# Optimization experiments

Hardware: AMD Instinct MI355X
Metric: run time of the kernel (lower is better)

## Reference

```python
import jax, jax.numpy as jnp
import numpy as np

B, C, H, W = 4, 128, 128, 128
SPHERE_SIZE, NUM_VOTES, NUM_PTS = 32768, 32, 4096
HW = H * W


def setup_inputs() -> dict:
    key = jax.random.key(0)
    k1, k2, k3, k4 = jax.random.split(key, 4)
    x = jax.random.normal(k1, (B, C, H, W), dtype=jnp.float32)
    vote_index = jax.random.randint(k2, (SPHERE_SIZE, NUM_VOTES), 0, HW, dtype=jnp.int32)
    vote_weight = jax.random.uniform(k3, (SPHERE_SIZE, NUM_VOTES), dtype=jnp.float32)
    inds = jax.random.randint(k4, (B, NUM_PTS), 0, SPHERE_SIZE, dtype=jnp.int64)
    return {"x": x, "vote_index": vote_index, "vote_weight": vote_weight, "inds": inds}


def reference(x, vote_index, vote_weight, inds):
    b, c, h, w = x.shape
    xf = x.reshape(b, c, h * w)                      # [B, C, HW]
    idx = jnp.take(vote_index, inds, axis=0)          # [B, P, V] flat HT indices
    wts = jnp.take(vote_weight, inds, axis=0)         # [B, P, V] vote weights

    def per_batch(xb, ib, wb):
        # xb: [C, HW], ib/wb: [P, V]
        g = jnp.take(xb, ib, axis=1)                  # [C, P, V] gather
        return jnp.einsum('cpv,pv->cp', g, wb)        # weighted vote accumulation

    return jax.vmap(per_batch)(xf, idx, wts)          # [B, C, P]
```

## Files before the change

### kernel.cpp

```cpp
#include <hip/hip_runtime.h>

constexpr int BB  = 4;
constexpr int CC  = 128;
constexpr int HWW = 16384;
constexpr int NV  = 32;
constexpr int NP  = 4096;
constexpr int PT  = 8;
constexpr int GT  = 128;

__global__ __launch_bounds__(256) void transpose_k(const float* __restrict__ x,
                                                   float* __restrict__ xt) {
  __shared__ float tile[32][33];
  const int b   = blockIdx.z;
  const int hw0 = blockIdx.x * 32;
  const int c0  = blockIdx.y * 32;
  const int tx  = threadIdx.x;
  const int ty  = threadIdx.y;
  const float* xb  = x  + (size_t)b * CC * HWW;
  float*       xtb = xt + (size_t)b * HWW * CC;
#pragma unroll
  for (int j = 0; j < 4; ++j)
    tile[ty + j * 8][tx] = xb[(size_t)(c0 + ty + j * 8) * HWW + hw0 + tx];
  __syncthreads();
#pragma unroll
  for (int j = 0; j < 4; ++j)
    xtb[(size_t)(hw0 + ty + j * 8) * CC + c0 + tx] = tile[tx][ty + j * 8];
}

__global__ __launch_bounds__(GT, 4) void gather_k(const float* __restrict__ xt,
                                                  const int* __restrict__ vote_index,
                                                  const float* __restrict__ vote_weight,
                                                  const int* __restrict__ inds,
                                                  float* __restrict__ out) {
  const int b   = blockIdx.y;
  const int p0  = blockIdx.x * PT;
  const int tid = threadIdx.x;
  const int sg  = tid >> 5;
  const int c4  = tid & 31;

  __shared__ int   s_idx[PT][NV];
  __shared__ float s_w[PT][NV];

#pragma unroll
  for (int i = tid; i < PT * NV; i += GT) {
    const int pp = i >> 5;
    const int v  = i & (NV - 1);
    const int s  = inds[b * NP + p0 + pp];
    s_idx[pp][v] = vote_index[s * NV + v] * CC;
    s_w[pp][v]   = vote_weight[s * NV + v];
  }
  __syncthreads();

  const float* xb = xt + (size_t)b * HWW * CC + (c4 << 2);

  float4 acc[2];
#pragma unroll
  for (int q = 0; q < 2; ++q) {
    const int pp = sg + q * 4;
    float4 a = {0.f, 0.f, 0.f, 0.f};
#pragma unroll
    for (int v = 0; v < NV; ++v) {
      const float  w  = s_w[pp][v];
      const float4 xv = *reinterpret_cast<const float4*>(xb + s_idx[pp][v]);
      a.x += xv.x * w;
      a.y += xv.y * w;
      a.z += xv.z * w;
      a.w += xv.w * w;
    }
    acc[q] = a;
  }
  __syncthreads();

  __shared__ float s_out[CC][PT + 4];
#pragma unroll
  for (int q = 0; q < 2; ++q) {
    const int pp = sg + q * 4;
    s_out[(c4 << 2) + 0][pp] = acc[q].x;
    s_out[(c4 << 2) + 1][pp] = acc[q].y;
    s_out[(c4 << 2) + 2][pp] = acc[q].z;
    s_out[(c4 << 2) + 3][pp] = acc[q].w;
  }
  __syncthreads();

  float* ob = out + ((size_t)b * CC + tid) * NP + p0;
  const float4 o0 = {s_out[tid][0], s_out[tid][1], s_out[tid][2], s_out[tid][3]};
  const float4 o1 = {s_out[tid][4], s_out[tid][5], s_out[tid][6], s_out[tid][7]};
  *reinterpret_cast<float4*>(ob)     = o0;
  *reinterpret_cast<float4*>(ob + 4) = o1;
}

__global__ __launch_bounds__(128) void gather_fallback_k(const float* __restrict__ x,
                                                         const int* __restrict__ vote_index,
                                                         const float* __restrict__ vote_weight,
                                                         const int* __restrict__ inds,
                                                         float* __restrict__ out) {
  const int b = blockIdx.y;
  const int p = blockIdx.x;
  const int c = threadIdx.x;
  const int s = inds[b * NP + p];
  const float* xb = x + ((size_t)b * CC + c) * HWW;
  float a = 0.f;
  for (int v = 0; v < NV; ++v)
    a += xb[vote_index[s * NV + v]] * vote_weight[s * NV + v];
  out[((size_t)b * CC + c) * NP + p] = a;
}

extern "C" void kernel_launch(void* const* d_in, const int* in_sizes, int n_in,
                              void* d_out, int out_size, void* d_ws, size_t ws_size,
                              hipStream_t stream) {
  const float* x           = (const float*)d_in[0];
  const int*   vote_index  = (const int*)d_in[1];
  const float* vote_weight = (const float*)d_in[2];
  const int*   inds        = (const int*)d_in[3];
  float*       out         = (float*)d_out;

  const size_t xt_bytes = (size_t)BB * HWW * CC * sizeof(float);
  if (ws_size >= xt_bytes) {
    float* xt = (float*)d_ws;
    dim3 tg(HWW / 32, CC / 32, BB);
    transpose_k<<<tg, dim3(32, 8), 0, stream>>>(x, xt);
    dim3 gg(NP / PT, BB);
    gather_k<<<gg, GT, 0, stream>>>(xt, vote_index, vote_weight, inds, out);
  } else {
    dim3 gg(NP, BB);
    gather_fallback_k<<<gg, CC, 0, stream>>>(x, vote_index, vote_weight, inds, out);
  }
}
```

Before: 120.1 us.

## Store transposed feature map in fp16 and gather 8 channels per load

The transpose kernel now writes the channel-last copy of x as fp16 and uses 64x64 tiles. The gather kernel reads 16-byte half8 vectors covering 8 channels per thread, so each thread handles one point instead of two. Halving the intermediate buffer cuts write traffic in the transpose and gather traffic in the second kernel. The trade-off is that x is rounded to fp16 before accumulation, which loses precision and changes results relative to the fp32 reference.

```diff
diff --git a/kernel.cpp b/kernel.cpp
--- a/kernel.cpp
+++ b/kernel.cpp
@@ -1,4 +1,8 @@
 #include <hip/hip_runtime.h>
+
+typedef _Float16 half_t;
+typedef _Float16 half2_t __attribute__((ext_vector_type(2)));
+typedef _Float16 half8_t __attribute__((ext_vector_type(8)));
 
 constexpr int BB  = 4;
 constexpr int CC  = 128;
@@ -8,26 +12,31 @@
 constexpr int PT  = 8;
 constexpr int GT  = 128;
 
-__global__ __launch_bounds__(256) void transpose_k(const float* __restrict__ x,
-                                                   float* __restrict__ xt) {
-  __shared__ float tile[32][33];
+__global__ __launch_bounds__(256) void transpose_h(const float* __restrict__ x,
+                                                   half_t* __restrict__ xt) {
+  __shared__ float tile[64][65];
   const int b   = blockIdx.z;
-  const int hw0 = blockIdx.x * 32;
-  const int c0  = blockIdx.y * 32;
-  const int tx  = threadIdx.x;
-  const int ty  = threadIdx.y;
-  const float* xb  = x  + (size_t)b * CC * HWW;
-  float*       xtb = xt + (size_t)b * HWW * CC;
+  const int hw0 = blockIdx.x * 64;
+  const int c0  = blockIdx.y * 64;
+  const int tx  = threadIdx.x & 63;
+  const int ty  = threadIdx.x >> 6;
+  const float* xb = x + (size_t)b * CC * HWW;
 #pragma unroll
-  for (int j = 0; j < 4; ++j)
-    tile[ty + j * 8][tx] = xb[(size_t)(c0 + ty + j * 8) * HWW + hw0 + tx];
+  for (int j = 0; j < 16; ++j)
+    tile[ty + j * 4][tx] = xb[(size_t)(c0 + ty + j * 4) * HWW + hw0 + tx];
   __syncthreads();
+  half_t* xtb = xt + (size_t)b * HWW * CC;
+  const int cp = threadIdx.x & 31;
+  const int r0 = threadIdx.x >> 5;
 #pragma unroll
-  for (int j = 0; j < 4; ++j)
-    xtb[(size_t)(hw0 + ty + j * 8) * CC + c0 + tx] = tile[tx][ty + j * 8];
+  for (int j = 0; j < 8; ++j) {
+    const int hwr = r0 + j * 8;
+    half2_t hv = {(half_t)tile[2 * cp][hwr], (half_t)tile[2 * cp + 1][hwr]};
+    *reinterpret_cast<half2_t*>(xtb + (size_t)(hw0 + hwr) * CC + c0 + 2 * cp) = hv;
+  }
 }
 
-__global__ __launch_bounds__(GT, 4) void gather_k(const float* __restrict__ xt,
+__global__ __launch_bounds__(GT, 4) void gather_h(const half_t* __restrict__ xt,
                                                   const int* __restrict__ vote_index,
                                                   const float* __restrict__ vote_weight,
                                                   const int* __restrict__ inds,
@@ -35,12 +44,11 @@
   const int b   = blockIdx.y;
   const int p0  = blockIdx.x * PT;
   const int tid = threadIdx.x;
-  const int sg  = tid >> 5;
-  const int c4  = tid & 31;
+  const int sg  = tid >> 4;
+  const int c8  = tid & 15;
 
   __shared__ int   s_idx[PT][NV];
   __shared__ float s_w[PT][NV];
-
 #pragma unroll
   for (int i = tid; i < PT * NV; i += GT) {
     const int pp = i >> 5;
@@ -51,40 +59,26 @@
   }
   __syncthreads();
 
-  const float* xb = xt + (size_t)b * HWW * CC + (c4 << 2);
+  const half_t* xb = xt + (size_t)b * HWW * CC + c8 * 8;
 
-  float4 acc[2];
+  float acc[8] = {0.f, 0.f, 0.f, 0.f, 0.f, 0.f, 0.f, 0.f};
 #pragma unroll
-  for (int q = 0; q < 2; ++q) {
-    const int pp = sg + q * 4;
-    float4 a = {0.f, 0.f, 0.f, 0.f};
+  for (int v = 0; v < NV; ++v) {
+    const half8_t xv = *reinterpret_cast<const half8_t*>(xb + s_idx[sg][v]);
+    const float   w  = s_w[sg][v];
 #pragma unroll
-    for (int v = 0; v < NV; ++v) {
-      const float  w  = s_w[pp][v];
-      const float4 xv = *reinterpret_cast<const float4*>(xb + s_idx[pp][v]);
-      a.x += xv.x * w;
-      a.y += xv.y * w;
-      a.z += xv.z * w;
-      a.w += xv.w * w;
-    }
-    acc[q] = a;
+    for (int k = 0; k < 8; ++k) acc[k] += (float)xv[k] * w;
   }
   __syncthreads();
 
-  __shared__ float s_out[CC][PT + 4];
+  __shared__ float s_out[PT][CC + 4];
 #pragma unroll
-  for (int q = 0; q < 2; ++q) {
-    const int pp = sg + q * 4;
-    s_out[(c4 << 2) + 0][pp] = acc[q].x;
-    s_out[(c4 << 2) + 1][pp] = acc[q].y;
-    s_out[(c4 << 2) + 2][pp] = acc[q].z;
-    s_out[(c4 << 2) + 3][pp] = acc[q].w;
-  }
+  for (int k = 0; k < 8; ++k) s_out[sg][c8 * 8 + k] = acc[k];
   __syncthreads();
 
   float* ob = out + ((size_t)b * CC + tid) * NP + p0;
-  const float4 o0 = {s_out[tid][0], s_out[tid][1], s_out[tid][2], s_out[tid][3]};
-  const float4 o1 = {s_out[tid][4], s_out[tid][5], s_out[tid][6], s_out[tid][7]};
+  const float4 o0 = {s_out[0][tid], s_out[1][tid], s_out[2][tid], s_out[3][tid]};
+  const float4 o1 = {s_out[4][tid], s_out[5][tid], s_out[6][tid], s_out[7][tid]};
   *reinterpret_cast<float4*>(ob)     = o0;
   *reinterpret_cast<float4*>(ob + 4) = o1;
 }
@@ -114,13 +108,13 @@
   const int*   inds        = (const int*)d_in[3];
   float*       out         = (float*)d_out;
 
-  const size_t xt_bytes = (size_t)BB * HWW * CC * sizeof(float);
+  const size_t xt_bytes = (size_t)BB * HWW * CC * sizeof(half_t);
   if (ws_size >= xt_bytes) {
-    float* xt = (float*)d_ws;
-    dim3 tg(HWW / 32, CC / 32, BB);
-    transpose_k<<<tg, dim3(32, 8), 0, stream>>>(x, xt);
+    half_t* xt = (half_t*)d_ws;
+    dim3 tg(HWW / 64, CC / 64, BB);
+    transpose_h<<<tg, 256, 0, stream>>>(x, xt);
     dim3 gg(NP / PT, BB);
-    gather_k<<<gg, GT, 0, stream>>>(xt, vote_index, vote_weight, inds, out);
+    gather_h<<<gg, GT, 0, stream>>>(xt, vote_index, vote_weight, inds, out);
   } else {
     dim3 gg(NP, BB);
     gather_fallback_k<<<gg, CC, 0, stream>>>(x, vote_index, vote_weight, inds, out);
```

Result: faster. 102.1 us (-15.0%).
